# Kernel tuning notes

Hardware: AMD Instinct MI355X
Metric: run time of the kernel (lower is better)

Reference implementation:

```python
import jax, jax.numpy as jnp
import numpy as np

N_NODES = 100000


def _mean_agg(x, src, dst, n_nodes):
    # gather source features along edges, segment-sum into destinations, divide by in-degree
    msg = x[src]                                               # [E, D]
    s = jax.ops.segment_sum(msg, dst, num_segments=n_nodes)    # [N, D]
    deg = jax.ops.segment_sum(jnp.ones((src.shape[0],), x.dtype), dst, num_segments=n_nodes)
    return s / jnp.maximum(deg, 1.0)[:, None]


def _sage_layer(x, src, dst, W_self, W_neigh, b, n_nodes):
    h_neigh = _mean_agg(x, src, dst, n_nodes)
    return x @ W_self + h_neigh @ W_neigh + b


def setup_inputs() -> dict:
    key = jax.random.key(0)
    ks = jax.random.split(key, 8)
    in_f, h_f, n_cls = 128, 128, 40
    n_edges = 1600000
    sc = lambda d: 1.0 / np.sqrt(d)
    return {
        "features": jax.random.normal(ks[0], (N_NODES, in_f), dtype=jnp.float32),
        "src": jax.random.randint(ks[1], (n_edges,), 0, N_NODES),
        "dst": jax.random.randint(ks[2], (n_edges,), 0, N_NODES),
        "W1_self": jax.random.normal(ks[3], (in_f, h_f), dtype=jnp.float32) * sc(in_f),
        "W1_neigh": jax.random.normal(ks[4], (in_f, h_f), dtype=jnp.float32) * sc(in_f),
        "b1": jnp.zeros((h_f,), dtype=jnp.float32),
        "W2_self": jax.random.normal(ks[5], (h_f, n_cls), dtype=jnp.float32) * sc(h_f),
        "W2_neigh": jax.random.normal(ks[6], (h_f, n_cls), dtype=jnp.float32) * sc(h_f),
        "b2": jnp.zeros((n_cls,), dtype=jnp.float32),
    }


def reference(features, src, dst, W1_self, W1_neigh, b1, W2_self, W2_neigh, b2):
    h = _sage_layer(features, src, dst, W1_self, W1_neigh, b1, N_NODES)
    h = jax.nn.relu(h)
    h = _sage_layer(h, src, dst, W2_self, W2_neigh, b2, N_NODES)
    return h
```

## Files before the change

kernel.cpp:

```cpp
#include <hip/hip_runtime.h>


typedef __attribute__((ext_vector_type(8))) short bf16x8;
typedef __attribute__((ext_vector_type(4))) float f32x4;
typedef __attribute__((ext_vector_type(2))) float f32x2;

#define BIN_SHIFT 7
#define BIN_SIZE  128
#define NB        256

#define OFF_ROWSTART (1ull << 20)
#define OFF_HIST     (2ull << 20)
#define OFF_SCAN     (3ull << 20)
#define OFF_BSUMS    (4ull << 20)
#define OFF_BOFFS    ((4ull << 20) + (64ull << 10))
#define OFF_PACKED   (5ull << 20)
#define OFF_CSR      (12ull << 20)
#define OFF_W1T      (19ull << 20)
#define OFF_W2T      (20ull << 20)
#define OFF_XB       (21ull << 20)
#define OFF_XQ       (47ull << 20)
#define OFF_AGGB     (61ull << 20)
#define OFF_T2LO     (87ull << 20)
#define OFF_T2HI     (94ull << 20)

static __device__ __forceinline__ unsigned short f2b(float f) {
    unsigned int u = __float_as_uint(f);
    u += 0x7fffu + ((u >> 16) & 1u);
    return (unsigned short)(u >> 16);
}
static __device__ __forceinline__ float blo(unsigned int v) { return __uint_as_float(v << 16); }
static __device__ __forceinline__ float bhi(unsigned int v) { return __uint_as_float(v & 0xffff0000u); }


__global__ __launch_bounds__(256) void cast_hist(
    const float* __restrict__ x,
    const float* __restrict__ W1s, const float* __restrict__ W1n,
    const float* __restrict__ W2s, const float* __restrict__ W2n,
    unsigned short* __restrict__ xb, unsigned char* __restrict__ xq,
    unsigned short* __restrict__ W1t, unsigned short* __restrict__ W2t,
    unsigned short* __restrict__ t2lo, unsigned short* __restrict__ t2hi,
    const int* __restrict__ dst, int* __restrict__ hist,
    int n16, int castBlocks, int castPlus, int N, int E, int nbins) {
    __shared__ int h[1024];
    int blk = blockIdx.x, t = threadIdx.x;
    if (blk >= castPlus) {
        int b = blk - castPlus;
        for (int i = t; i < nbins; i += 256) h[i] = 0;
        __syncthreads();
        int chunk = (E + NB - 1) / NB;
        int base = b * chunk;
        int lim = min(base + chunk, E);
        for (int e = base + t; e < lim; e += 256)
            atomicAdd(&h[dst[e] >> BIN_SHIFT], 1);
        __syncthreads();
        for (int i = t; i < nbins; i += 256)
            hist[i * NB + b] = h[i];
        return;
    }
    if (blk < castBlocks) {
        int i = blk * 256 + t;
        if (i >= n16) return;
        const float4* p = (const float4*)x + (size_t)i * 4;
        float4 v0 = p[0], v1 = p[1], v2 = p[2], v3 = p[3];
        float f[16] = {v0.x, v0.y, v0.z, v0.w, v1.x, v1.y, v1.z, v1.w,
                       v2.x, v2.y, v2.z, v2.w, v3.x, v3.y, v3.z, v3.w};
        unsigned short ob[16];
#pragma unroll
        for (int k = 0; k < 16; k++) ob[k] = f2b(f[k]);
        *(float4*)(xb + (size_t)i * 16) = *(float4*)&ob[0];
        *(float4*)(xb + (size_t)i * 16 + 8) = *(float4*)&ob[8];
        unsigned int w[4];
#pragma unroll
        for (int k = 0; k < 4; k++) {
            int u = __builtin_amdgcn_cvt_pk_fp8_f32(f[4 * k + 0], f[4 * k + 1], 0, false);
            u = __builtin_amdgcn_cvt_pk_fp8_f32(f[4 * k + 2], f[4 * k + 3], u, true);
            w[k] = (unsigned int)u;
        }
        *(uint4*)(xq + (size_t)i * 16) = *(uint4*)w;
    } else if (blk < castBlocks + 128) {
        int c = blk - castBlocks;
        float v = (t < 128) ? W1s[(size_t)t * 128 + c] : W1n[(size_t)(t - 128) * 128 + c];
        W1t[(size_t)c * 256 + t] = f2b(v);
    } else if (blk < castBlocks + 208) {
        if (t < 128) {
            int c = blk - castBlocks - 128;
            float v = (c < 40) ? W2s[(size_t)t * 40 + c] : W2n[(size_t)t * 40 + (c - 40)];
            W2t[(size_t)c * 128 + t] = f2b(v);
        }
    } else {
        if (t < 32) ((unsigned int*)(xq + (size_t)N * 128))[t] = 0u;
        else if (t < 48) ((unsigned int*)(t2lo + (size_t)N * 32))[t - 32] = 0u;
        else if (t < 52) ((unsigned int*)(t2hi + (size_t)N * 8))[t - 48] = 0u;
    }
}


__global__ void scan1(const int* __restrict__ in, int* __restrict__ tmp,
                      int* __restrict__ bsums, int M) {
    __shared__ int s[256];
    int t = threadIdx.x;
    int i = blockIdx.x * 256 + t;
    int v = (i < M) ? in[i] : 0;
    s[t] = v;
    __syncthreads();
    for (int off = 1; off < 256; off <<= 1) {
        int u = (t >= off) ? s[t - off] : 0;
        __syncthreads();
        s[t] += u;
        __syncthreads();
    }
    if (i < M) tmp[i] = s[t] - v;
    if (t == 255) bsums[blockIdx.x] = s[t];
}

__global__ void scan2(const int* __restrict__ bsums, int* __restrict__ boffs, int nb) {
    __shared__ int s[1024];
    int t = threadIdx.x;
    int v = (t < nb) ? bsums[t] : 0;
    s[t] = v;
    __syncthreads();
    for (int off = 1; off < 1024; off <<= 1) {
        int u = (t >= off) ? s[t - off] : 0;
        __syncthreads();
        s[t] += u;
        __syncthreads();
    }
    if (t < nb) boffs[t] = s[t] - v;
}

__global__ __launch_bounds__(256) void scatter_det(
    const int* __restrict__ src, const int* __restrict__ dst,
    const int* __restrict__ tmp, const int* __restrict__ boffs,
    unsigned int* __restrict__ packed, int E, int nbins) {
    __shared__ int cur[1024];
    int b = blockIdx.x, t = threadIdx.x;
    for (int i = t; i < nbins; i += 256) cur[i] = tmp[i * NB + b] + boffs[i];
    __syncthreads();
    int chunk = (E + NB - 1) / NB;
    int base = b * chunk;
    int lim = min(base + chunk, E);
    for (int e = base + t; e < lim; e += 256) {
        int d = dst[e];
        int bin = d >> BIN_SHIFT;
        int pos = atomicAdd(&cur[bin], 1);
        packed[pos] = ((unsigned int)(d & (BIN_SIZE - 1)) << 20) | (unsigned int)src[e];
    }
}

__global__ __launch_bounds__(256) void bin_fill(
    const unsigned int* __restrict__ packed, const int* __restrict__ tmp,
    const int* __restrict__ boffs,
    int* __restrict__ row_start, int* __restrict__ csr_src, int N, int nbins, int E) {
    __shared__ int cnt[BIN_SIZE];
    __shared__ int pre[BIN_SIZE];
    __shared__ int ex[BIN_SIZE];
    int b = blockIdx.x;
    int t = threadIdx.x;
    int node0 = b << BIN_SHIFT;
    int beg = tmp[b * NB] + boffs[b];
    int end = (b + 1 < nbins) ? (tmp[(b + 1) * NB] + boffs[b + 1]) : E;

    if (t < BIN_SIZE) cnt[t] = 0;
    __syncthreads();
    for (int i = beg + t; i < end; i += 256)
        atomicAdd(&cnt[packed[i] >> 20], 1);
    __syncthreads();
    if (t < BIN_SIZE) pre[t] = cnt[t];
    __syncthreads();
    for (int off = 1; off < BIN_SIZE; off <<= 1) {
        int u = (t < BIN_SIZE && t >= off) ? pre[t - off] : 0;
        __syncthreads();
        if (t < BIN_SIZE) pre[t] += u;
        __syncthreads();
    }
    if (t < BIN_SIZE) {
        ex[t] = pre[t] - cnt[t];
        int node = node0 + t;
        if (node < N) row_start[node] = beg + ex[t];
        cnt[t] = 0;
    }
    if (b == nbins - 1 && t == 0) row_start[N] = E;
    __syncthreads();
    for (int i = beg + t; i < end; i += 256) {
        unsigned int p = packed[i];
        int dl = p >> 20;
        int s = p & 0xFFFFF;
        int ofs = atomicAdd(&cnt[dl], 1);
        csr_src[beg + ex[dl] + ofs] = s;
    }
}


__global__ void agg_mean_fp8(const unsigned char* __restrict__ xq,
                             const int* __restrict__ row_start,
                             const int* __restrict__ csr_src,
                             unsigned short* __restrict__ aggb, int N) {
    int wv = (blockIdx.x * blockDim.x + threadIdx.x) >> 6;
    int lane = threadIdx.x & 63;
    if (2 * wv >= N) return;
    int node = 2 * wv + (lane >> 5);
    bool valid = node < N;
    int hl = lane & 31;
    int g = hl >> 4;
    int l = hl & 15;
    int beg = valid ? row_start[node] : 0;
    int end = valid ? row_start[node + 1] : 0;
    const char* xbase = (const char*)xq;
    unsigned loff = (unsigned)l << 3;

    float a[8];
#pragma unroll
    for (int k = 0; k < 8; k++) a[k] = 0.f;

    for (int e = beg; e < end; e += 16) {
        int s[8];
#pragma unroll
        for (int k = 0; k < 8; k++) {
            int ee = e + 2 * k + g;
            int idx = csr_src[min(ee, end - 1)];
            s[k] = (ee < end) ? idx : N;
        }
#pragma unroll
        for (int k = 0; k < 8; k++) {
            uint2 v = *(const uint2*)(xbase + (((unsigned)s[k] << 7) + loff));
            f32x2 p0 = __builtin_amdgcn_cvt_pk_f32_fp8(v.x, false);
            f32x2 p1 = __builtin_amdgcn_cvt_pk_f32_fp8(v.x, true);
            f32x2 p2 = __builtin_amdgcn_cvt_pk_f32_fp8(v.y, false);
            f32x2 p3 = __builtin_amdgcn_cvt_pk_f32_fp8(v.y, true);
            a[0] += p0.x; a[1] += p0.y; a[2] += p1.x; a[3] += p1.y;
            a[4] += p2.x; a[5] += p2.y; a[6] += p3.x; a[7] += p3.y;
        }
    }

#pragma unroll
    for (int k = 0; k < 8; k++)
        a[k] += __shfl_xor(a[k], 16);
    if (g == 0 && valid) {
        float inv = 1.0f / fmaxf((float)(end - beg), 1.0f);
        unsigned int ow[4];
#pragma unroll
        for (int k = 0; k < 4; k++)
            ow[k] = (unsigned int)f2b(a[2 * k] * inv) |
                    ((unsigned int)f2b(a[2 * k + 1] * inv) << 16);
        *(uint4*)((char*)aggb + (((unsigned)node << 8) + ((unsigned)l << 4))) = *(uint4*)ow;
    }
}

__global__ void agg2_add(const unsigned short* __restrict__ t2lo,
                         const unsigned short* __restrict__ t2hi,
                         const int* __restrict__ row_start,
                         const int* __restrict__ csr_src, const float* __restrict__ b2,
                         float* __restrict__ out, int N) {
    int wv = (blockIdx.x * blockDim.x + threadIdx.x) >> 6;
    int lane = threadIdx.x & 63;
    if (2 * wv >= N) return;
    int node = 2 * wv + (lane >> 5);
    bool valid = node < N;
    int hl = lane & 31;
    int g = hl >> 4;
    int l = hl & 15;
    int beg = valid ? row_start[node] : 0;
    int end = valid ? row_start[node + 1] : 0;
    const char* lob = (const char*)t2lo;
    const char* hib = (const char*)t2hi;
    bool isLo = (l < 8);
    bool active = (l < 10);
    unsigned loff = isLo ? ((unsigned)l << 3) : ((unsigned)(l - 8) << 3);

    float a0 = 0.f, a1 = 0.f, a2 = 0.f, a3 = 0.f;

    for (int e = beg; e < end; e += 16) {
        int s[8];
#pragma unroll
        for (int k = 0; k < 8; k++) {
            int ee = e + 2 * k + g;
            int idx = csr_src[min(ee, end - 1)];
            s[k] = (ee < end) ? idx : N;
        }
        if (active) {
#pragma unroll
            for (int k = 0; k < 8; k++) {
                uint2 v = isLo ? *(const uint2*)(lob + (((unsigned)s[k] << 6) + loff))
                               : *(const uint2*)(hib + (((unsigned)s[k] << 4) + loff));
                a0 += blo(v.x); a1 += bhi(v.x);
                a2 += blo(v.y); a3 += bhi(v.y);
            }
        }
    }

    a0 += __shfl_xor(a0, 16);
    a1 += __shfl_xor(a1, 16);
    a2 += __shfl_xor(a2, 16);
    a3 += __shfl_xor(a3, 16);
    if (g == 0 && active && valid) {
        float inv = 1.0f / fmaxf((float)(end - beg), 1.0f);
        float4 bb = ((const float4*)b2)[l];
        float4* op = (float4*)((char*)out + ((unsigned)node * 160u + ((unsigned)l << 4)));
        float4 cur = *op;
        cur.x += a0 * inv + bb.x;
        cur.y += a1 * inv + bb.y;
        cur.z += a2 * inv + bb.z;
        cur.w += a3 * inv + bb.w;
        *op = cur;
    }
}


__global__ __launch_bounds__(256) void gemm12_mfma(
    const unsigned short* __restrict__ xb, const unsigned short* __restrict__ aggb,
    const unsigned short* __restrict__ W1t, const unsigned short* __restrict__ W2t,
    const float* __restrict__ b1, float* __restrict__ out,
    unsigned short* __restrict__ t2lo, unsigned short* __restrict__ t2hi, int N) {

    __shared__ unsigned short As[128 * 40];
    __shared__ unsigned short Bs[128 * 40];
    __shared__ unsigned short Hs[128 * 136];
    __shared__ unsigned short B2[80 * 136];

    int tid = threadIdx.x;
    int wave = tid >> 6, lane = tid & 63;
    int row0 = blockIdx.x * 128;
    int m = lane & 15, quad = lane >> 4;

    for (int idx = tid; idx < 1280; idx += 256) {
        int r = idx >> 4, seg = idx & 15;
        *(float4*)&B2[r * 136 + seg * 8] = *(const float4*)(W2t + (size_t)r * 128 + seg * 8);
    }

    f32x4 acc[2][8];
#pragma unroll
    for (int i = 0; i < 2; i++)
#pragma unroll
        for (int j = 0; j < 8; j++) acc[i][j] = (f32x4){0.f, 0.f, 0.f, 0.f};

    for (int k0 = 0; k0 < 256; k0 += 32) {
        __syncthreads();
        {
            int r = tid >> 1, kk = (tid & 1) * 16;
            int row = row0 + r;
            float4 v0 = make_float4(0, 0, 0, 0), v1 = v0;
            if (row < N) {
                const unsigned short* s = (k0 < 128)
                    ? (xb + (size_t)row * 128 + k0 + kk)
                    : (aggb + (size_t)row * 128 + (k0 - 128) + kk);
                const float4* p = (const float4*)s;
                v0 = p[0]; v1 = p[1];
            }
            *(float4*)&As[r * 40 + kk] = v0;
            *(float4*)&As[r * 40 + kk + 8] = v1;
            const float4* q2 = (const float4*)(W1t + (size_t)r * 256 + k0 + kk);
            float4 w0 = q2[0], w1 = q2[1];
            *(float4*)&Bs[r * 40 + kk] = w0;
            *(float4*)&Bs[r * 40 + kk + 8] = w1;
        }
        __syncthreads();

        bf16x8 af0 = *(bf16x8*)&As[(wave * 32 + m) * 40 + quad * 8];
        bf16x8 af1 = *(bf16x8*)&As[(wave * 32 + 16 + m) * 40 + quad * 8];
#pragma unroll
        for (int j = 0; j < 8; j++) {
            bf16x8 bfg = *(bf16x8*)&Bs[(j * 16 + m) * 40 + quad * 8];
            acc[0][j] = __builtin_amdgcn_mfma_f32_16x16x32_bf16(af0, bfg, acc[0][j], 0, 0, 0);
            acc[1][j] = __builtin_amdgcn_mfma_f32_16x16x32_bf16(af1, bfg, acc[1][j], 0, 0, 0);
        }
    }

#pragma unroll
    for (int j = 0; j < 8; j++) {
        int col = j * 16 + m;
        float bias = b1[col];
#pragma unroll
        for (int i = 0; i < 2; i++) {
#pragma unroll
            for (int r = 0; r < 4; r++) {
                int rl = wave * 32 + i * 16 + quad * 4 + r;
                Hs[rl * 136 + col] = f2b(fmaxf(acc[i][j][r] + bias, 0.f));
            }
        }
    }
    __syncthreads();

    f32x4 acc2[2][5];
#pragma unroll
    for (int i = 0; i < 2; i++)
#pragma unroll
        for (int j = 0; j < 5; j++) acc2[i][j] = (f32x4){0.f, 0.f, 0.f, 0.f};

#pragma unroll
    for (int k0 = 0; k0 < 128; k0 += 32) {
        bf16x8 af0 = *(bf16x8*)&Hs[(wave * 32 + m) * 136 + k0 + quad * 8];
        bf16x8 af1 = *(bf16x8*)&Hs[(wave * 32 + 16 + m) * 136 + k0 + quad * 8];
#pragma unroll
        for (int j = 0; j < 5; j++) {
            bf16x8 bfg = *(bf16x8*)&B2[(j * 16 + m) * 136 + k0 + quad * 8];
            acc2[0][j] = __builtin_amdgcn_mfma_f32_16x16x32_bf16(af0, bfg, acc2[0][j], 0, 0, 0);
            acc2[1][j] = __builtin_amdgcn_mfma_f32_16x16x32_bf16(af1, bfg, acc2[1][j], 0, 0, 0);
        }
    }

#pragma unroll
    for (int j = 0; j < 5; j++) {
        int col = j * 16 + m;
#pragma unroll
        for (int i = 0; i < 2; i++) {
#pragma unroll
            for (int r = 0; r < 4; r++) {
                int row = row0 + wave * 32 + i * 16 + quad * 4 + r;
                if (row < N) {
                    float v = acc2[i][j][r];
                    if (col < 40) {
                        out[(size_t)row * 40 + col] = v;
                    } else {
                        int td = col - 40;
                        if (td < 32) t2lo[(size_t)row * 32 + td] = f2b(v);
                        else         t2hi[(size_t)row * 8 + (td - 32)] = f2b(v);
                    }
                }
            }
        }
    }
}


extern "C" void kernel_launch(void* const* d_in, const int* in_sizes, int n_in,
                              void* d_out, int out_size, void* d_ws, size_t ws_size,
                              hipStream_t stream) {
    const float* x   = (const float*)d_in[0];
    const int*   src = (const int*)d_in[1];
    const int*   dst = (const int*)d_in[2];
    const float* W1s = (const float*)d_in[3];
    const float* W1n = (const float*)d_in[4];
    const float* b1  = (const float*)d_in[5];
    const float* W2s = (const float*)d_in[6];
    const float* W2n = (const float*)d_in[7];
    const float* b2  = (const float*)d_in[8];
    float* out = (float*)d_out;

    int N = in_sizes[0] / 128;
    int E = in_sizes[1];
    int nbins = (N + BIN_SIZE - 1) / BIN_SIZE;
    int M = nbins * NB;

    char* ws = (char*)d_ws;
    int*            row_start  = (int*)(ws + OFF_ROWSTART);
    int*            hist       = (int*)(ws + OFF_HIST);
    int*            scanned    = (int*)(ws + OFF_SCAN);
    int*            bsums      = (int*)(ws + OFF_BSUMS);
    int*            boffs      = (int*)(ws + OFF_BOFFS);
    unsigned int*   packed     = (unsigned int*)(ws + OFF_PACKED);
    int*            csr_src    = (int*)(ws + OFF_CSR);
    unsigned short* W1t        = (unsigned short*)(ws + OFF_W1T);
    unsigned short* W2t        = (unsigned short*)(ws + OFF_W2T);
    unsigned short* xb         = (unsigned short*)(ws + OFF_XB);
    unsigned char*  xq         = (unsigned char*)(ws + OFF_XQ);
    unsigned short* aggb       = (unsigned short*)(ws + OFF_AGGB);
    unsigned short* t2lo       = (unsigned short*)(ws + OFF_T2LO);
    unsigned short* t2hi       = (unsigned short*)(ws + OFF_T2HI);

    int scanBlocks = (M + 255) / 256;

    int n16 = N * 128 / 16;
    int castBlocks = (n16 + 255) / 256;
    int castPlus = castBlocks + 128 + 80 + 1;

    cast_hist<<<castPlus + NB, 256, 0, stream>>>(
        x, W1s, W1n, W2s, W2n, xb, xq, W1t, W2t, t2lo, t2hi,
        dst, hist, n16, castBlocks, castPlus, N, E, nbins);
    scan1<<<scanBlocks, 256, 0, stream>>>(hist, scanned, bsums, M);
    scan2<<<1, 1024, 0, stream>>>(bsums, boffs, scanBlocks);
    scatter_det<<<NB, 256, 0, stream>>>(src, dst, scanned, boffs, packed, E, nbins);
    bin_fill<<<nbins, 256, 0, stream>>>(packed, scanned, boffs, row_start, csr_src, N, nbins, E);

    int nodePairs = (N + 1) / 2;
    int aggBlocks = (nodePairs * 64 + 255) / 256;
    agg_mean_fp8<<<aggBlocks, 256, 0, stream>>>(xq, row_start, csr_src, aggb, N);
    gemm12_mfma<<<(N + 127) / 128, 256, 0, stream>>>(xb, aggb, W1t, W2t, b1, out, t2lo, t2hi, N);
    agg2_add<<<aggBlocks, 256, 0, stream>>>(t2lo, t2hi, row_start, csr_src, b2, out, N);
}
```

Baseline: 273.9 us.

## Fuse first-layer mean aggregation into the layer-1 GEMM kernel via shared memory

```diff
diff --git a/kernel.cpp b/kernel.cpp
--- a/kernel.cpp
+++ b/kernel.cpp
@@ -20,7 +20,6 @@
 #define OFF_W2T      (20ull << 20)
 #define OFF_XB       (21ull << 20)
 #define OFF_XQ       (47ull << 20)
-#define OFF_AGGB     (61ull << 20)
 #define OFF_T2LO     (87ull << 20)
 #define OFF_T2HI     (94ull << 20)
 
@@ -191,61 +190,6 @@
     }
 }
 
-
-__global__ void agg_mean_fp8(const unsigned char* __restrict__ xq,
-                             const int* __restrict__ row_start,
-                             const int* __restrict__ csr_src,
-                             unsigned short* __restrict__ aggb, int N) {
-    int wv = (blockIdx.x * blockDim.x + threadIdx.x) >> 6;
-    int lane = threadIdx.x & 63;
-    if (2 * wv >= N) return;
-    int node = 2 * wv + (lane >> 5);
-    bool valid = node < N;
-    int hl = lane & 31;
-    int g = hl >> 4;
-    int l = hl & 15;
-    int beg = valid ? row_start[node] : 0;
-    int end = valid ? row_start[node + 1] : 0;
-    const char* xbase = (const char*)xq;
-    unsigned loff = (unsigned)l << 3;
-
-    float a[8];
-#pragma unroll
-    for (int k = 0; k < 8; k++) a[k] = 0.f;
-
-    for (int e = beg; e < end; e += 16) {
-        int s[8];
-#pragma unroll
-        for (int k = 0; k < 8; k++) {
-            int ee = e + 2 * k + g;
-            int idx = csr_src[min(ee, end - 1)];
-            s[k] = (ee < end) ? idx : N;
-        }
-#pragma unroll
-        for (int k = 0; k < 8; k++) {
-            uint2 v = *(const uint2*)(xbase + (((unsigned)s[k] << 7) + loff));
-            f32x2 p0 = __builtin_amdgcn_cvt_pk_f32_fp8(v.x, false);
-            f32x2 p1 = __builtin_amdgcn_cvt_pk_f32_fp8(v.x, true);
-            f32x2 p2 = __builtin_amdgcn_cvt_pk_f32_fp8(v.y, false);
-            f32x2 p3 = __builtin_amdgcn_cvt_pk_f32_fp8(v.y, true);
-            a[0] += p0.x; a[1] += p0.y; a[2] += p1.x; a[3] += p1.y;
-            a[4] += p2.x; a[5] += p2.y; a[6] += p3.x; a[7] += p3.y;
-        }
-    }
-
-#pragma unroll
-    for (int k = 0; k < 8; k++)
-        a[k] += __shfl_xor(a[k], 16);
-    if (g == 0 && valid) {
-        float inv = 1.0f / fmaxf((float)(end - beg), 1.0f);
-        unsigned int ow[4];
-#pragma unroll
-        for (int k = 0; k < 4; k++)
-            ow[k] = (unsigned int)f2b(a[2 * k] * inv) |
-                    ((unsigned int)f2b(a[2 * k + 1] * inv) << 16);
-        *(uint4*)((char*)aggb + (((unsigned)node << 8) + ((unsigned)l << 4))) = *(uint4*)ow;
-    }
-}
 
 __global__ void agg2_add(const unsigned short* __restrict__ t2lo,
                          const unsigned short* __restrict__ t2hi,
@@ -308,9 +252,11 @@
 
 
 __global__ __launch_bounds__(256) void gemm12_mfma(
-    const unsigned short* __restrict__ xb, const unsigned short* __restrict__ aggb,
+    const unsigned short* __restrict__ xb, const unsigned char* __restrict__ xq,
     const unsigned short* __restrict__ W1t, const unsigned short* __restrict__ W2t,
-    const float* __restrict__ b1, float* __restrict__ out,
+    const float* __restrict__ b1,
+    const int* __restrict__ row_start, const int* __restrict__ csr_src,
+    float* __restrict__ out,
     unsigned short* __restrict__ t2lo, unsigned short* __restrict__ t2hi, int N) {
 
     __shared__ unsigned short As[128 * 40];
@@ -328,6 +274,55 @@
         *(float4*)&B2[r * 136 + seg * 8] = *(const float4*)(W2t + (size_t)r * 128 + seg * 8);
     }
 
+    {
+        int hl = lane & 31;
+        int g = hl >> 4;
+        int l = hl & 15;
+        const char* xbase = (const char*)xq;
+        unsigned loff = (unsigned)l << 3;
+        for (int p = 0; p < 16; p++) {
+            int nl = wave * 32 + p * 2 + (lane >> 5);
+            int node = row0 + nl;
+            bool valid = node < N;
+            int beg = valid ? row_start[node] : 0;
+            int end = valid ? row_start[node + 1] : 0;
+            float a[8];
+#pragma unroll
+            for (int k = 0; k < 8; k++) a[k] = 0.f;
+            for (int e = beg; e < end; e += 16) {
+                int s[8];
+#pragma unroll
+                for (int k = 0; k < 8; k++) {
+                    int ee = e + 2 * k + g;
+                    int idx = csr_src[min(ee, end - 1)];
+                    s[k] = (ee < end) ? idx : N;
+                }
+#pragma unroll
+                for (int k = 0; k < 8; k++) {
+                    uint2 v = *(const uint2*)(xbase + (((unsigned)s[k] << 7) + loff));
+                    f32x2 p0 = __builtin_amdgcn_cvt_pk_f32_fp8(v.x, false);
+                    f32x2 p1 = __builtin_amdgcn_cvt_pk_f32_fp8(v.x, true);
+                    f32x2 p2 = __builtin_amdgcn_cvt_pk_f32_fp8(v.y, false);
+                    f32x2 p3 = __builtin_amdgcn_cvt_pk_f32_fp8(v.y, true);
+                    a[0] += p0.x; a[1] += p0.y; a[2] += p1.x; a[3] += p1.y;
+                    a[4] += p2.x; a[5] += p2.y; a[6] += p3.x; a[7] += p3.y;
+                }
+            }
+#pragma unroll
+            for (int k = 0; k < 8; k++)
+                a[k] += __shfl_xor(a[k], 16);
+            if (g == 0) {
+                float inv = 1.0f / fmaxf((float)(end - beg), 1.0f);
+#pragma unroll
+                for (int j = 0; j < 4; j++) {
+                    unsigned int u = (unsigned int)f2b(a[2 * j] * inv) |
+                                     ((unsigned int)f2b(a[2 * j + 1] * inv) << 16);
+                    *(unsigned int*)&Hs[nl * 136 + l * 8 + 2 * j] = u;
+                }
+            }
+        }
+    }
+
     f32x4 acc[2][8];
 #pragma unroll
     for (int i = 0; i < 2; i++)
@@ -339,16 +334,15 @@
         {
             int r = tid >> 1, kk = (tid & 1) * 16;
             int row = row0 + r;
-            float4 v0 = make_float4(0, 0, 0, 0), v1 = v0;
-            if (row < N) {
-                const unsigned short* s = (k0 < 128)
-                    ? (xb + (size_t)row * 128 + k0 + kk)
-                    : (aggb + (size_t)row * 128 + (k0 - 128) + kk);
-                const float4* p = (const float4*)s;
-                v0 = p[0]; v1 = p[1];
-            }
-            *(float4*)&As[r * 40 + kk] = v0;
-            *(float4*)&As[r * 40 + kk + 8] = v1;
+            if (k0 < 128) {
+                float4 v0 = make_float4(0, 0, 0, 0), v1 = v0;
+                if (row < N) {
+                    const float4* p = (const float4*)(xb + (size_t)row * 128 + k0 + kk);
+                    v0 = p[0]; v1 = p[1];
+                }
+                *(float4*)&As[r * 40 + kk] = v0;
+                *(float4*)&As[r * 40 + kk + 8] = v1;
+            }
             const float4* q2 = (const float4*)(W1t + (size_t)r * 256 + k0 + kk);
             float4 w0 = q2[0], w1 = q2[1];
             *(float4*)&Bs[r * 40 + kk] = w0;
@@ -356,8 +350,15 @@
         }
         __syncthreads();
 
-        bf16x8 af0 = *(bf16x8*)&As[(wave * 32 + m) * 40 + quad * 8];
-        bf16x8 af1 = *(bf16x8*)&As[(wave * 32 + 16 + m) * 40 + quad * 8];
+        bf16x8 af0, af1;
+        if (k0 < 128) {
+            af0 = *(bf16x8*)&As[(wave * 32 + m) * 40 + quad * 8];
+            af1 = *(bf16x8*)&As[(wave * 32 + 16 + m) * 40 + quad * 8];
+        } else {
+            int aoff = (k0 - 128) + quad * 8;
+            af0 = *(bf16x8*)&Hs[(wave * 32 + m) * 136 + aoff];
+            af1 = *(bf16x8*)&Hs[(wave * 32 + 16 + m) * 136 + aoff];
+        }
 #pragma unroll
         for (int j = 0; j < 8; j++) {
             bf16x8 bfg = *(bf16x8*)&Bs[(j * 16 + m) * 40 + quad * 8];
@@ -454,7 +455,6 @@
     unsigned short* W2t        = (unsigned short*)(ws + OFF_W2T);
     unsigned short* xb         = (unsigned short*)(ws + OFF_XB);
     unsigned char*  xq         = (unsigned char*)(ws + OFF_XQ);
-    unsigned short* aggb       = (unsigned short*)(ws + OFF_AGGB);
     unsigned short* t2lo       = (unsigned short*)(ws + OFF_T2LO);
     unsigned short* t2hi       = (unsigned short*)(ws + OFF_T2HI);
 
@@ -472,9 +472,10 @@
     scatter_det<<<NB, 256, 0, stream>>>(src, dst, scanned, boffs, packed, E, nbins);
     bin_fill<<<nbins, 256, 0, stream>>>(packed, scanned, boffs, row_start, csr_src, N, nbins, E);
 
+    gemm12_mfma<<<(N + 127) / 128, 256, 0, stream>>>(
+        xb, xq, W1t, W2t, b1, row_start, csr_src, out, t2lo, t2hi, N);
+
     int nodePairs = (N + 1) / 2;
     int aggBlocks = (nodePairs * 64 + 255) / 256;
-    agg_mean_fp8<<<aggBlocks, 256, 0, stream>>>(xq, row_start, csr_src, aggb, N);
-    gemm12_mfma<<<(N + 127) / 128, 256, 0, stream>>>(xb, aggb, W1t, W2t, b1, out, t2lo, t2hi, N);
     agg2_add<<<aggBlocks, 256, 0, stream>>>(t2lo, t2hi, row_start, csr_src, b2, out, N);
 }
```

New measurement: 310.2 us. 1.13x slower.

## Compute per-node degrees in histogram pass and derive row_start via global scan

Applied to the files above, without the earlier changes.

```diff
diff --git a/kernel.cpp b/kernel.cpp
--- a/kernel.cpp
+++ b/kernel.cpp
@@ -10,10 +10,14 @@
 #define NB        256
 
 #define OFF_ROWSTART (1ull << 20)
+#define OFF_SCAND    ((1ull << 20) + (512ull << 10))
 #define OFF_HIST     (2ull << 20)
 #define OFF_SCAN     (3ull << 20)
 #define OFF_BSUMS    (4ull << 20)
 #define OFF_BOFFS    ((4ull << 20) + (64ull << 10))
+#define OFF_BSUMS2   ((4ull << 20) + (128ull << 10))
+#define OFF_BOFFS2   ((4ull << 20) + (192ull << 10))
+#define OFF_DEG      ((4ull << 20) + (256ull << 10))
 #define OFF_PACKED   (5ull << 20)
 #define OFF_CSR      (12ull << 20)
 #define OFF_W1T      (19ull << 20)
@@ -40,7 +44,7 @@
     unsigned short* __restrict__ xb, unsigned char* __restrict__ xq,
     unsigned short* __restrict__ W1t, unsigned short* __restrict__ W2t,
     unsigned short* __restrict__ t2lo, unsigned short* __restrict__ t2hi,
-    const int* __restrict__ dst, int* __restrict__ hist,
+    const int* __restrict__ dst, int* __restrict__ hist, int* __restrict__ deg,
     int n16, int castBlocks, int castPlus, int N, int E, int nbins) {
     __shared__ int h[1024];
     int blk = blockIdx.x, t = threadIdx.x;
@@ -51,8 +55,11 @@
         int chunk = (E + NB - 1) / NB;
         int base = b * chunk;
         int lim = min(base + chunk, E);
-        for (int e = base + t; e < lim; e += 256)
-            atomicAdd(&h[dst[e] >> BIN_SHIFT], 1);
+        for (int e = base + t; e < lim; e += 256) {
+            int d = dst[e];
+            atomicAdd(&h[d >> BIN_SHIFT], 1);
+            atomicAdd(&deg[d], 1);
+        }
         __syncthreads();
         for (int i = t; i < nbins; i += 256)
             hist[i * NB + b] = h[i];
@@ -114,10 +121,14 @@
     if (t == 255) bsums[blockIdx.x] = s[t];
 }
 
-__global__ void scan2(const int* __restrict__ bsums, int* __restrict__ boffs, int nb) {
+__global__ void scan2(const int* __restrict__ bsums1, int* __restrict__ boffs1, int nb1,
+                      const int* __restrict__ bsums2, int* __restrict__ boffs2, int nb2) {
     __shared__ int s[1024];
+    const int* in = (blockIdx.x == 0) ? bsums1 : bsums2;
+    int* outp = (blockIdx.x == 0) ? boffs1 : boffs2;
+    int nb = (blockIdx.x == 0) ? nb1 : nb2;
     int t = threadIdx.x;
-    int v = (t < nb) ? bsums[t] : 0;
+    int v = (t < nb) ? in[t] : 0;
     s[t] = v;
     __syncthreads();
     for (int off = 1; off < 1024; off <<= 1) {
@@ -126,7 +137,14 @@
         s[t] += u;
         __syncthreads();
     }
-    if (t < nb) boffs[t] = s[t] - v;
+    if (t < nb) outp[t] = s[t] - v;
+}
+
+__global__ void finish_rs(const int* __restrict__ scand, const int* __restrict__ boffs2,
+                          int* __restrict__ row_start, int N, int E) {
+    int i = blockIdx.x * 256 + threadIdx.x;
+    if (i < N) row_start[i] = scand[i] + boffs2[i >> 8];
+    if (i == N) row_start[N] = E;
 }
 
 __global__ __launch_bounds__(256) void scatter_det(
@@ -148,46 +166,28 @@
     }
 }
 
-__global__ __launch_bounds__(256) void bin_fill(
-    const unsigned int* __restrict__ packed, const int* __restrict__ tmp,
-    const int* __restrict__ boffs,
-    int* __restrict__ row_start, int* __restrict__ csr_src, int N, int nbins, int E) {
+__global__ __launch_bounds__(256) void bin_fill_lite(
+    const unsigned int* __restrict__ packed, const int* __restrict__ row_start,
+    int* __restrict__ csr_src, int N, int nbins, int E) {
+    __shared__ int rs[BIN_SIZE];
     __shared__ int cnt[BIN_SIZE];
-    __shared__ int pre[BIN_SIZE];
-    __shared__ int ex[BIN_SIZE];
     int b = blockIdx.x;
     int t = threadIdx.x;
     int node0 = b << BIN_SHIFT;
-    int beg = tmp[b * NB] + boffs[b];
-    int end = (b + 1 < nbins) ? (tmp[(b + 1) * NB] + boffs[b + 1]) : E;
-
-    if (t < BIN_SIZE) cnt[t] = 0;
+    if (t < BIN_SIZE) {
+        int node = node0 + t;
+        rs[t] = row_start[min(node, N)];
+        cnt[t] = 0;
+    }
     __syncthreads();
-    for (int i = beg + t; i < end; i += 256)
-        atomicAdd(&cnt[packed[i] >> 20], 1);
-    __syncthreads();
-    if (t < BIN_SIZE) pre[t] = cnt[t];
-    __syncthreads();
-    for (int off = 1; off < BIN_SIZE; off <<= 1) {
-        int u = (t < BIN_SIZE && t >= off) ? pre[t - off] : 0;
-        __syncthreads();
-        if (t < BIN_SIZE) pre[t] += u;
-        __syncthreads();
-    }
-    if (t < BIN_SIZE) {
-        ex[t] = pre[t] - cnt[t];
-        int node = node0 + t;
-        if (node < N) row_start[node] = beg + ex[t];
-        cnt[t] = 0;
-    }
-    if (b == nbins - 1 && t == 0) row_start[N] = E;
-    __syncthreads();
+    int beg = rs[0];
+    int end = (b + 1 < nbins) ? row_start[min(node0 + BIN_SIZE, N)] : E;
     for (int i = beg + t; i < end; i += 256) {
         unsigned int p = packed[i];
         int dl = p >> 20;
         int s = p & 0xFFFFF;
         int ofs = atomicAdd(&cnt[dl], 1);
-        csr_src[beg + ex[dl] + ofs] = s;
+        csr_src[rs[dl] + ofs] = s;
     }
 }
 
@@ -444,10 +444,14 @@
 
     char* ws = (char*)d_ws;
     int*            row_start  = (int*)(ws + OFF_ROWSTART);
+    int*            scand      = (int*)(ws + OFF_SCAND);
     int*            hist       = (int*)(ws + OFF_HIST);
     int*            scanned    = (int*)(ws + OFF_SCAN);
     int*            bsums      = (int*)(ws + OFF_BSUMS);
     int*            boffs      = (int*)(ws + OFF_BOFFS);
+    int*            bsums2     = (int*)(ws + OFF_BSUMS2);
+    int*            boffs2     = (int*)(ws + OFF_BOFFS2);
+    int*            deg        = (int*)(ws + OFF_DEG);
     unsigned int*   packed     = (unsigned int*)(ws + OFF_PACKED);
     int*            csr_src    = (int*)(ws + OFF_CSR);
     unsigned short* W1t        = (unsigned short*)(ws + OFF_W1T);
@@ -458,19 +462,24 @@
     unsigned short* t2lo       = (unsigned short*)(ws + OFF_T2LO);
     unsigned short* t2hi       = (unsigned short*)(ws + OFF_T2HI);
 
-    int scanBlocks = (M + 255) / 256;
+    int scanBlocksM = (M + 255) / 256;
+    int scanBlocksN = (N + 255) / 256;
 
     int n16 = N * 128 / 16;
     int castBlocks = (n16 + 255) / 256;
     int castPlus = castBlocks + 128 + 80 + 1;
 
+    hipMemsetAsync(deg, 0, (size_t)(N + 1) * sizeof(int), stream);
+
     cast_hist<<<castPlus + NB, 256, 0, stream>>>(
         x, W1s, W1n, W2s, W2n, xb, xq, W1t, W2t, t2lo, t2hi,
-        dst, hist, n16, castBlocks, castPlus, N, E, nbins);
-    scan1<<<scanBlocks, 256, 0, stream>>>(hist, scanned, bsums, M);
-    scan2<<<1, 1024, 0, stream>>>(bsums, boffs, scanBlocks);
+        dst, hist, deg, n16, castBlocks, castPlus, N, E, nbins);
+    scan1<<<scanBlocksM, 256, 0, stream>>>(hist, scanned, bsums, M);
+    scan1<<<scanBlocksN, 256, 0, stream>>>(deg, scand, bsums2, N);
+    scan2<<<2, 1024, 0, stream>>>(bsums, boffs, scanBlocksM, bsums2, boffs2, scanBlocksN);
+    finish_rs<<<scanBlocksN + 1, 256, 0, stream>>>(scand, boffs2, row_start, N, E);
     scatter_det<<<NB, 256, 0, stream>>>(src, dst, scanned, boffs, packed, E, nbins);
-    bin_fill<<<nbins, 256, 0, stream>>>(packed, scanned, boffs, row_start, csr_src, N, nbins, E);
+    bin_fill_lite<<<nbins, 256, 0, stream>>>(packed, row_start, csr_src, N, nbins, E);
 
     int nodePairs = (N + 1) / 2;
     int aggBlocks = (nodePairs * 64 + 255) / 256;
```

Result: slower. 341.8 us (+24.8%).
